# Optimization experiments

Measured on AMD Instinct MI355X. Metric: run time of the kernel, lower is better.

Reference implementation:

```python
import jax, jax.numpy as jnp
import numpy as np

HIDDEN = 512
HEADS = 8
HEAD_DIM = HIDDEN // HEADS


def setup_inputs() -> dict:
    key = jax.random.key(0)
    ks = jax.random.split(key, 9)
    B, S = 4, 2048
    scale = 1.0 / np.sqrt(HIDDEN)
    x = jax.random.normal(ks[0], (B, S, HIDDEN), dtype=jnp.float32)
    Wq = jax.random.normal(ks[1], (HIDDEN, HIDDEN), dtype=jnp.float32) * scale
    Wk = jax.random.normal(ks[2], (HIDDEN, HIDDEN), dtype=jnp.float32) * scale
    Wv = jax.random.normal(ks[3], (HIDDEN, HIDDEN), dtype=jnp.float32) * scale
    Wo = jax.random.normal(ks[4], (HIDDEN, HIDDEN), dtype=jnp.float32) * scale
    bq = jax.random.normal(ks[5], (HIDDEN,), dtype=jnp.float32) * 0.01
    bk = jax.random.normal(ks[6], (HIDDEN,), dtype=jnp.float32) * 0.01
    bv = jax.random.normal(ks[7], (HIDDEN,), dtype=jnp.float32) * 0.01
    bo = jax.random.normal(ks[8], (HIDDEN,), dtype=jnp.float32) * 0.01
    return {"x": x, "Wq": Wq, "bq": bq, "Wk": Wk, "bk": bk,
            "Wv": Wv, "bv": bv, "Wo": Wo, "bo": bo}


def reference(x, Wq, bq, Wk, bk, Wv, bv, Wo, bo):
    B, S, _ = x.shape
    # project and split heads: [B, H, S, D]
    def split_heads(t):
        return t.reshape(B, S, HEADS, HEAD_DIM).transpose(0, 2, 1, 3)
    Q = split_heads(x @ Wq.T + bq)
    K = split_heads(x @ Wk.T + bk)
    V = split_heads(x @ Wv.T + bv)
    scores = jnp.einsum("bhsd,bhtd->bhst", Q, K) / jnp.sqrt(
        jnp.array(HEAD_DIM, dtype=x.dtype))
    attn = jax.nn.softmax(scores, axis=-1)  # dropout is identity in eval
    ctx = jnp.einsum("bhst,bhtd->bhsd", attn, V)
    ctx = ctx.transpose(0, 2, 1, 3).reshape(B, S, HIDDEN)
    return ctx @ Wo.T + bo
```

## Files before the change

### kernel.cpp

```cpp
#include <hip/hip_runtime.h>
#include <stdint.h>

#define HID 512
#define NH 8
#define HD 64
#define BB 4
#define SS 2048

typedef unsigned short u16;
typedef __attribute__((ext_vector_type(8))) short short8;
typedef __attribute__((ext_vector_type(4))) float f32x4;
typedef __attribute__((ext_vector_type(4))) _Float16 f16x4;
typedef __attribute__((ext_vector_type(2))) unsigned int uint2v;

#define MFMA16(a, b, c) __builtin_amdgcn_mfma_f32_16x16x32_bf16((a), (b), (c), 0, 0, 0)
#define MFMAH16(a, b, c) __builtin_amdgcn_mfma_f32_16x16x16f16((a), (b), (c), 0, 0, 0)

#define WAIT_VM4() __builtin_amdgcn_s_waitcnt(0xF74)
#define WAIT_VM3() __builtin_amdgcn_s_waitcnt(0xF73)
#define WAIT_VM0() __builtin_amdgcn_s_waitcnt(0xF70)
#define PIPE_BARRIER() do { asm volatile("" ::: "memory"); \
  __builtin_amdgcn_s_barrier(); asm volatile("" ::: "memory"); } while (0)

__device__ __forceinline__ u16 f2bf(float f) {
  union { float f; uint32_t u; } v; v.f = f;
  return (u16)((v.u + 0x7fffu + ((v.u >> 16) & 1u)) >> 16);
}

__device__ __forceinline__ u16 f2h(float f) {
  _Float16 h = (_Float16)f;
  return __builtin_bit_cast(u16, h);
}

__device__ __forceinline__ void gl_lds16(const u16* g, u16* l) {
  __builtin_amdgcn_global_load_lds(
      (const __attribute__((address_space(1))) unsigned int*)g,
      (__attribute__((address_space(3))) unsigned int*)l, 16, 0, 0);
}

__global__ void prep(const float* __restrict__ x,
                     const float* __restrict__ w0, const float* __restrict__ w1,
                     const float* __restrict__ w2, const float* __restrict__ w3,
                     u16* __restrict__ xb,
                     u16* __restrict__ o0, u16* __restrict__ o1,
                     u16* __restrict__ o2, u16* __restrict__ o3) {
  const int bid = blockIdx.x;
  const float* in;
  u16* out;
  int base;
  if (bid < 4096) {
    in = x; out = xb; base = bid * 1024;
  } else {
    const int z = (bid - 4096) >> 8;
    base = ((bid - 4096) & 255) * 1024;
    in = (z == 0) ? w0 : (z == 1) ? w1 : (z == 2) ? w2 : w3;
    out = (z == 0) ? o0 : (z == 1) ? o1 : (z == 2) ? o2 : o3;
  }
  const int i = base + threadIdx.x * 4;
  float4 v = *(const float4*)(in + i);
  ushort4 o;
  o.x = f2bf(v.x); o.y = f2bf(v.y); o.z = f2bf(v.z); o.w = f2bf(v.w);
  *(ushort4*)(out + i) = o;
}

__global__ __launch_bounds__(256, 3)
void qkv_gemm(const u16* __restrict__ xb,
              const u16* __restrict__ wq, const u16* __restrict__ wk, const u16* __restrict__ wv,
              const float* __restrict__ bq, const float* __restrict__ bk, const float* __restrict__ bv,
              u16* __restrict__ Q, u16* __restrict__ K, u16* __restrict__ Vt) {
  __shared__ u16 sA[3][4096];
  __shared__ u16 sB[3][4096];
  const int tid = threadIdx.x;
  const int lane = tid & 63;
  const int wave = tid >> 6;
  const int l15 = lane & 15;
  const int quad = lane >> 4;
  const int wm = wave >> 1, wn = wave & 1;

  const int L = blockIdx.x;
  const int xcd = L & 7;
  const int slot = L >> 3;
  const int bm = xcd * 8 + (slot & 7);
  const int r2 = slot >> 3;
  const int bn = r2 & 3;
  const int z = r2 >> 2;

  const float* bias = (z == 0) ? bq : (z == 1) ? bk : bv;
  const float scale = (z == 0) ? 0.18033688011112042f : 1.0f;

  const u16* Arows = (z == 2) ? wv : xb;
  const u16* Brows = (z == 2) ? xb : ((z == 0) ? wq : wk);
  const int am0 = (z == 2) ? (bn * 128) : (bm * 128);
  const int bn0 = (z == 2) ? (bm * 128) : (bn * 128);

  const int srow = tid >> 2;
  const int sg = (tid & 3) ^ ((srow >> 1) & 3);
  const u16* gA = Arows + (am0 + srow) * 512 + sg * 8;
  const u16* gB = Brows + (bn0 + srow) * 512 + sg * 8;

  const int fsw = (quad ^ ((l15 >> 1) & 3)) * 8;
  int aoff[4], boff[4];
#pragma unroll
  for (int t = 0; t < 4; ++t) {
    aoff[t] = (wm * 64 + t * 16 + l15) * 32 + fsw;
    boff[t] = (wn * 64 + t * 16 + l15) * 32 + fsw;
  }

  f32x4 acc[4][4] = {};

#pragma unroll
  for (int t = 0; t < 2; ++t) {
    const int k0 = t * 32;
    gl_lds16(gA + k0, &sA[t][wave * 512]);
    gl_lds16(gA + k0 + 64 * 512, &sA[t][2048 + wave * 512]);
    gl_lds16(gB + k0, &sB[t][wave * 512]);
    gl_lds16(gB + k0 + 64 * 512, &sB[t][2048 + wave * 512]);
  }

  for (int kk = 0; kk < 16; ++kk) {
    WAIT_VM4();
    PIPE_BARRIER();
    {
      const int tp = (kk + 2 < 16) ? kk + 2 : 15;
      const int ns = (kk + 2) % 3;
      const int k0 = tp * 32;
      gl_lds16(gA + k0, &sA[ns][wave * 512]);
      gl_lds16(gA + k0 + 64 * 512, &sA[ns][2048 + wave * 512]);
      gl_lds16(gB + k0, &sB[ns][wave * 512]);
      gl_lds16(gB + k0 + 64 * 512, &sB[ns][2048 + wave * 512]);
    }
    const int cur = kk % 3;
    short8 af[4], bf[4];
#pragma unroll
    for (int t = 0; t < 4; ++t) af[t] = *(const short8*)&sA[cur][aoff[t]];
#pragma unroll
    for (int t = 0; t < 4; ++t) bf[t] = *(const short8*)&sB[cur][boff[t]];
#pragma unroll
    for (int mi = 0; mi < 4; ++mi)
#pragma unroll
      for (int ni = 0; ni < 4; ++ni)
        acc[mi][ni] = MFMA16(af[mi], bf[ni], acc[mi][ni]);
  }

  if (z != 2) {
    u16* dst = (z == 0) ? Q : K;
#pragma unroll
    for (int mi = 0; mi < 4; ++mi) {
#pragma unroll
      for (int ni = 0; ni < 4; ++ni) {
        const int col = bn0 + wn * 64 + ni * 16 + l15;
        const float bs = bias[col];
#pragma unroll
        for (int i = 0; i < 4; ++i) {
          const int row = am0 + wm * 64 + mi * 16 + quad * 4 + i;
          const float v = (acc[mi][ni][i] + bs) * scale;
          const int b = row >> 11, s = row & 2047;
          const int h = col >> 6, d = col & 63;
          dst[(((size_t)(b * 8 + h) * 2048 + s) << 6) + d] = f2bf(v);
        }
      }
    }
  } else {
#pragma unroll
    for (int mi = 0; mi < 4; ++mi) {
#pragma unroll
      for (int i = 0; i < 4; ++i) {
        const int o = am0 + wm * 64 + mi * 16 + quad * 4 + i;
        const float bs = bias[o];
        const int h = o >> 6, d = o & 63;
#pragma unroll
        for (int ni = 0; ni < 4; ++ni) {
          const int r = bn0 + wn * 64 + ni * 16 + l15;
          const int b = r >> 11, s = r & 2047;
          Vt[(((size_t)(b * 8 + h) * 64 + d) << 11) + s] = f2h(acc[mi][ni][i] + bs);
        }
      }
    }
  }
}

__global__ __launch_bounds__(512, 4)
void attn(const u16* __restrict__ Q, const u16* __restrict__ K,
          const u16* __restrict__ Vt, u16* __restrict__ ctx) {
  __shared__ __align__(16) u16 smem[4 * 8192];
  const int tid = threadIdx.x;
  const int lane = tid & 63;
  const int wave = tid >> 6;
  const int l15 = lane & 15;
  const int quad = lane >> 4;
  const int pair = wave >> 1;
  const int par = wave & 1;

  const int L = blockIdx.x;
  const int xcd = L & 7;
  const int slotb = L >> 3;
  const int bh = xcd * 4 + (slotb & 3);
  const int qt = slotb >> 2;

  const u16* Qb = Q + (size_t)bh * SS * HD;
  const u16* Kb = K + (size_t)bh * SS * HD;
  const u16* Vb = Vt + (size_t)bh * HD * SS;

  const int rowbase = qt * 128 + pair * 32;
  short8 qf[2][2];
#pragma unroll
  for (int rf = 0; rf < 2; ++rf)
#pragma unroll
    for (int kc = 0; kc < 2; ++kc)
      qf[rf][kc] = *(const short8*)(Qb + (rowbase + rf * 16 + l15) * 64 + kc * 32 + quad * 8);
  asm volatile("" ::: "memory");

  f32x4 oacc[2][4] = {};
  float plsum[2] = {0.f, 0.f};

  const int trow = tid >> 3;
  const int gsw = (tid & 7) ^ (trow & 7);
  const int kOff = trow * 64 + gsw * 8;
  const int vOff = trow * 2048 + gsw * 8;
  u16* ldsK = smem + tid * 8;
  u16* ldsV = smem + 4096 + tid * 8;

  const int l7 = l15 & 7;
  int kfo[2];
#pragma unroll
  for (int kc = 0; kc < 2; ++kc)
    kfo[kc] = (par * 32 + l15) * 64 + ((kc * 4 + quad) ^ l7) * 8;
  int vfo[2];
#pragma unroll
  for (int tb = 0; tb < 2; ++tb)
    vfo[tb] = l15 * 64 + (((par * 4 + tb * 2 + (quad >> 1)) ^ l7) * 8) + (quad & 1) * 4;

#pragma unroll
  for (int t = 0; t < 3; ++t) {
    gl_lds16(Kb + t * 4096 + kOff, ldsK + t * 8192);
    gl_lds16(Vb + t * 64 + vOff, ldsV + t * 8192);
  }

  for (int tt = 0; tt < 32; ++tt) {
    WAIT_VM4();
    PIPE_BARRIER();
    {
      const int tp = (tt + 3 < 32) ? tt + 3 : 31;
      const int ns = (tt + 3) & 3;
      gl_lds16(Kb + tp * 4096 + kOff, ldsK + ns * 8192);
      gl_lds16(Vb + tp * 64 + vOff, ldsV + ns * 8192);
    }
    const int cb = (tt & 3) * 8192;

#pragma unroll
    for (int tb = 0; tb < 2; ++tb) {
      const short8 k0 = *(const short8*)&smem[cb + tb * 1024 + kfo[0]];
      const short8 k1 = *(const short8*)&smem[cb + tb * 1024 + kfo[1]];
      f32x4 sacc[2] = {};
#pragma unroll
      for (int rf = 0; rf < 2; ++rf) {
        sacc[rf] = MFMA16(k0, qf[rf][0], sacc[rf]);
        sacc[rf] = MFMA16(k1, qf[rf][1], sacc[rf]);
      }
      uint2v vf[4];
#pragma unroll
      for (int nd = 0; nd < 4; ++nd)
        vf[nd] = *(const uint2v*)&smem[cb + 4096 + nd * 1024 + vfo[tb]];
#pragma unroll
      for (int rf = 0; rf < 2; ++rf) {
        const float p0 = __builtin_amdgcn_exp2f(sacc[rf][0]);
        const float p1 = __builtin_amdgcn_exp2f(sacc[rf][1]);
        const float p2 = __builtin_amdgcn_exp2f(sacc[rf][2]);
        const float p3 = __builtin_amdgcn_exp2f(sacc[rf][3]);
        plsum[rf] += (p0 + p1) + (p2 + p3);
        uint2v pu;
        pu.x = __builtin_bit_cast(unsigned int, __builtin_amdgcn_cvt_pkrtz(p0, p1));
        pu.y = __builtin_bit_cast(unsigned int, __builtin_amdgcn_cvt_pkrtz(p2, p3));
        const f16x4 pf = __builtin_bit_cast(f16x4, pu);
#pragma unroll
        for (int nd = 0; nd < 4; ++nd)
          oacc[rf][nd] = MFMAH16(pf, __builtin_bit_cast(f16x4, vf[nd]), oacc[rf][nd]);
      }
    }
  }

  WAIT_VM0();
  __syncthreads();

#pragma unroll
  for (int rf = 0; rf < 2; ++rf) {
    plsum[rf] += __shfl_xor(plsum[rf], 16);
    plsum[rf] += __shfl_xor(plsum[rf], 32);
  }

  float* cbuf = (float*)smem;
  float* lbuf = cbuf + 128 * 68;
  if (par) {
#pragma unroll
    for (int rf = 0; rf < 2; ++rf) {
#pragma unroll
      for (int nd = 0; nd < 4; ++nd)
#pragma unroll
        for (int i = 0; i < 4; ++i)
          cbuf[(pair * 32 + rf * 16 + quad * 4 + i) * 68 + nd * 16 + l15] = oacc[rf][nd][i];
      if (quad == 0) lbuf[pair * 32 + rf * 16 + l15] = plsum[rf];
    }
  }
  __syncthreads();
  if (!par) {
    const int b = bh >> 3, h = bh & 7;
#pragma unroll
    for (int rf = 0; rf < 2; ++rf) {
      const float tot = plsum[rf] + lbuf[pair * 32 + rf * 16 + l15];
      float inv[4];
#pragma unroll
      for (int i = 0; i < 4; ++i)
        inv[i] = __builtin_amdgcn_rcpf(__shfl(tot, quad * 4 + i));
#pragma unroll
      for (int nd = 0; nd < 4; ++nd)
#pragma unroll
        for (int i = 0; i < 4; ++i) {
          const float v = (oacc[rf][nd][i] +
                           cbuf[(pair * 32 + rf * 16 + quad * 4 + i) * 68 + nd * 16 + l15]) * inv[i];
          const int s = rowbase + rf * 16 + quad * 4 + i;
          const int d = nd * 16 + l15;
          ctx[((size_t)(b * 2048 + s) << 9) + h * 64 + d] = f2bf(v);
        }
    }
  }
}

__global__ __launch_bounds__(256, 2)
void out_gemm(const u16* __restrict__ A, const u16* __restrict__ W,
              const float* __restrict__ bias, float* __restrict__ out) {
  __shared__ u16 sA[3][4096];
  __shared__ u16 sB[3][2048];
  const int tid = threadIdx.x;
  const int lane = tid & 63;
  const int wave = tid >> 6;
  const int l15 = lane & 15;
  const int quad = lane >> 4;

  const int L = blockIdx.x;
  const int xcd = L & 7;
  const int slot = L >> 3;
  const int bm = xcd * 8 + (slot & 7);
  const int bn = slot >> 3;

  const int srow = tid >> 2;
  const int sg = (tid & 3) ^ ((srow >> 1) & 3);
  const u16* gA = A + (bm * 128 + srow) * 512 + sg * 8;
  const u16* gB = W + (bn * 64 + srow) * 512 + sg * 8;

  const int fsw = (quad ^ ((l15 >> 1) & 3)) * 8;
  int aoff[2], boff[4];
#pragma unroll
  for (int t = 0; t < 2; ++t) aoff[t] = (wave * 32 + t * 16 + l15) * 32 + fsw;
#pragma unroll
  for (int t = 0; t < 4; ++t) boff[t] = (t * 16 + l15) * 32 + fsw;

  f32x4 acc[2][4] = {};

#pragma unroll
  for (int t = 0; t < 2; ++t) {
    const int k0 = t * 32;
    gl_lds16(gA + k0, &sA[t][wave * 512]);
    gl_lds16(gA + k0 + 64 * 512, &sA[t][2048 + wave * 512]);
    gl_lds16(gB + k0, &sB[t][wave * 512]);
  }

  for (int kk = 0; kk < 16; ++kk) {
    WAIT_VM3();
    PIPE_BARRIER();
    {
      const int tp = (kk + 2 < 16) ? kk + 2 : 15;
      const int ns = (kk + 2) % 3;
      const int k0 = tp * 32;
      gl_lds16(gA + k0, &sA[ns][wave * 512]);
      gl_lds16(gA + k0 + 64 * 512, &sA[ns][2048 + wave * 512]);
      gl_lds16(gB + k0, &sB[ns][wave * 512]);
    }
    const int cur = kk % 3;
    short8 af[2], bf[4];
#pragma unroll
    for (int t = 0; t < 2; ++t) af[t] = *(const short8*)&sA[cur][aoff[t]];
#pragma unroll
    for (int t = 0; t < 4; ++t) bf[t] = *(const short8*)&sB[cur][boff[t]];
#pragma unroll
    for (int mi = 0; mi < 2; ++mi)
#pragma unroll
      for (int ni = 0; ni < 4; ++ni)
        acc[mi][ni] = MFMA16(af[mi], bf[ni], acc[mi][ni]);
  }

#pragma unroll
  for (int mi = 0; mi < 2; ++mi) {
#pragma unroll
    for (int ni = 0; ni < 4; ++ni) {
      const int col = bn * 64 + ni * 16 + l15;
      const float bs = bias[col];
#pragma unroll
      for (int i = 0; i < 4; ++i) {
        const int row = bm * 128 + wave * 32 + mi * 16 + quad * 4 + i;
        out[(size_t)row * 512 + col] = acc[mi][ni][i] + bs;
      }
    }
  }
}

extern "C" void kernel_launch(void* const* d_in, const int* in_sizes, int n_in,
                              void* d_out, int out_size, void* d_ws, size_t ws_size,
                              hipStream_t stream) {
  const float* x = (const float*)d_in[0];
  const float* Wq = (const float*)d_in[1];
  const float* bq = (const float*)d_in[2];
  const float* Wk = (const float*)d_in[3];
  const float* bk = (const float*)d_in[4];
  const float* Wv = (const float*)d_in[5];
  const float* bv = (const float*)d_in[6];
  const float* Wo = (const float*)d_in[7];
  const float* bo = (const float*)d_in[8];
  float* out = (float*)d_out;

  char* ws = (char*)d_ws;
  u16* xb  = (u16*)(ws);
  u16* wqb = (u16*)(ws + (8u << 20));
  u16* wkb = (u16*)(ws + (8u << 20) + (512u << 10));
  u16* wvb = (u16*)(ws + (9u << 20));
  u16* wob = (u16*)(ws + (9u << 20) + (512u << 10));
  u16* Qb  = (u16*)(ws + (10u << 20));
  u16* Kb  = (u16*)(ws + (18u << 20));
  u16* Vtb = (u16*)(ws + (26u << 20));
  u16* ctx = (u16*)(ws + (34u << 20));

  prep<<<5120, 256, 0, stream>>>(x, Wq, Wk, Wv, Wo, xb, wqb, wkb, wvb, wob);
  qkv_gemm<<<768, 256, 0, stream>>>(xb, wqb, wkb, wvb, bq, bk, bv, Qb, Kb, Vtb);
  attn<<<512, 512, 0, stream>>>(Qb, Kb, Vtb, ctx);
  out_gemm<<<512, 256, 0, stream>>>(ctx, wob, bo, out);
}
```

Baseline: 156.4 us.

## Restructure attention into per-wave K pipelines with V loaded into registers

```diff
diff --git a/kernel.cpp b/kernel.cpp
--- a/kernel.cpp
+++ b/kernel.cpp
@@ -19,8 +19,8 @@
 #define WAIT_VM4() __builtin_amdgcn_s_waitcnt(0xF74)
 #define WAIT_VM3() __builtin_amdgcn_s_waitcnt(0xF73)
 #define WAIT_VM0() __builtin_amdgcn_s_waitcnt(0xF70)
-#define PIPE_BARRIER() do { asm volatile("" ::: "memory"); \
-  __builtin_amdgcn_s_barrier(); asm volatile("" ::: "memory"); } while (0)
+#define FENCE() asm volatile("" ::: "memory")
+#define PIPE_BARRIER() do { FENCE(); __builtin_amdgcn_s_barrier(); FENCE(); } while (0)
 
 __device__ __forceinline__ u16 f2bf(float f) {
   union { float f; uint32_t u; } v; v.f = f;
@@ -179,10 +179,10 @@
   }
 }
 
-__global__ __launch_bounds__(512, 4)
+__global__ __launch_bounds__(256, 4)
 void attn(const u16* __restrict__ Q, const u16* __restrict__ K,
           const u16* __restrict__ Vt, u16* __restrict__ ctx) {
-  __shared__ __align__(16) u16 smem[4 * 8192];
+  __shared__ __align__(16) u16 smem[4 * 4096];
   const int tid = threadIdx.x;
   const int lane = tid & 63;
   const int wave = tid >> 6;
@@ -201,72 +201,83 @@
   const u16* Kb = K + (size_t)bh * SS * HD;
   const u16* Vb = Vt + (size_t)bh * HD * SS;
 
-  const int rowbase = qt * 128 + pair * 32;
+  const int rowbase = qt * 64 + pair * 32;
   short8 qf[2][2];
 #pragma unroll
   for (int rf = 0; rf < 2; ++rf)
 #pragma unroll
     for (int kc = 0; kc < 2; ++kc)
       qf[rf][kc] = *(const short8*)(Qb + (rowbase + rf * 16 + l15) * 64 + kc * 32 + quad * 8);
-  asm volatile("" ::: "memory");
 
   f32x4 oacc[2][4] = {};
   float plsum[2] = {0.f, 0.f};
 
-  const int trow = tid >> 3;
-  const int gsw = (tid & 7) ^ (trow & 7);
-  const int kOff = trow * 64 + gsw * 8;
-  const int vOff = trow * 2048 + gsw * 8;
-  u16* ldsK = smem + tid * 8;
-  u16* ldsV = smem + 4096 + tid * 8;
+  const int krho = lane >> 3;
+  const int kdg = (lane & 7) ^ krho;
+  const u16* ksrc = Kb + (par * 32 + krho) * 64 + kdg * 8;
+  u16* kdst = smem + wave * 4096 + lane * 8;
 
   const int l7 = l15 & 7;
-  int kfo[2];
-#pragma unroll
-  for (int kc = 0; kc < 2; ++kc)
-    kfo[kc] = (par * 32 + l15) * 64 + ((kc * 4 + quad) ^ l7) * 8;
-  int vfo[2];
+  int kfo[2][2];
 #pragma unroll
   for (int tb = 0; tb < 2; ++tb)
-    vfo[tb] = l15 * 64 + (((par * 4 + tb * 2 + (quad >> 1)) ^ l7) * 8) + (quad & 1) * 4;
-
-#pragma unroll
-  for (int t = 0; t < 3; ++t) {
-    gl_lds16(Kb + t * 4096 + kOff, ldsK + t * 8192);
-    gl_lds16(Vb + t * 64 + vOff, ldsV + t * 8192);
-  }
+#pragma unroll
+    for (int kc = 0; kc < 2; ++kc)
+      kfo[tb][kc] = wave * 4096 + (tb * 16 + l15) * 64 + ((kc * 4 + quad) ^ l7) * 8;
+
+  const u16* vsrc = Vb + l15 * 2048 + par * 32 + quad * 4;
+
+#define ISSUE_K(tile, slot)                                                   \
+  do {                                                                        \
+    _Pragma("unroll") for (int c = 0; c < 4; ++c)                             \
+      gl_lds16(ksrc + (size_t)(tile) * 4096 + c * 512,                        \
+               kdst + (slot) * 2048 + c * 512);                               \
+  } while (0)
+
+#define ISSUE_V(vreg, tile)                                                   \
+  do {                                                                        \
+    _Pragma("unroll") for (int tb = 0; tb < 2; ++tb)                          \
+      _Pragma("unroll") for (int nd = 0; nd < 4; ++nd)                        \
+        vreg[tb][nd] = *(const uint2v*)(vsrc + nd * 32768 + tb * 16 +         \
+                                        (size_t)(tile) * 64);                 \
+  } while (0)
+
+  uint2v vf[2][4];
+  ISSUE_K(0, 0);
+  ISSUE_K(1, 1);
+  ISSUE_V(vf, 0);
+  WAIT_VM0();
+  FENCE();
 
   for (int tt = 0; tt < 32; ++tt) {
-    WAIT_VM4();
-    PIPE_BARRIER();
-    {
-      const int tp = (tt + 3 < 32) ? tt + 3 : 31;
-      const int ns = (tt + 3) & 3;
-      gl_lds16(Kb + tp * 4096 + kOff, ldsK + ns * 8192);
-      gl_lds16(Vb + tp * 64 + vOff, ldsV + ns * 8192);
-    }
-    const int cb = (tt & 3) * 8192;
-
+    const int cs = (tt & 1) * 2048;
+
+    f32x4 sacc[2][2];
 #pragma unroll
     for (int tb = 0; tb < 2; ++tb) {
-      const short8 k0 = *(const short8*)&smem[cb + tb * 1024 + kfo[0]];
-      const short8 k1 = *(const short8*)&smem[cb + tb * 1024 + kfo[1]];
-      f32x4 sacc[2] = {};
+      const short8 k0 = *(const short8*)&smem[cs + kfo[tb][0]];
+      const short8 k1 = *(const short8*)&smem[cs + kfo[tb][1]];
 #pragma unroll
       for (int rf = 0; rf < 2; ++rf) {
-        sacc[rf] = MFMA16(k0, qf[rf][0], sacc[rf]);
-        sacc[rf] = MFMA16(k1, qf[rf][1], sacc[rf]);
+        f32x4 s = {};
+        s = MFMA16(k0, qf[rf][0], s);
+        s = MFMA16(k1, qf[rf][1], s);
+        sacc[tb][rf] = s;
       }
-      uint2v vf[4];
-#pragma unroll
-      for (int nd = 0; nd < 4; ++nd)
-        vf[nd] = *(const uint2v*)&smem[cb + 4096 + nd * 1024 + vfo[tb]];
+    }
+
+    FENCE();
+    WAIT_VM0();
+    FENCE();
+
+#pragma unroll
+    for (int tb = 0; tb < 2; ++tb) {
 #pragma unroll
       for (int rf = 0; rf < 2; ++rf) {
-        const float p0 = __builtin_amdgcn_exp2f(sacc[rf][0]);
-        const float p1 = __builtin_amdgcn_exp2f(sacc[rf][1]);
-        const float p2 = __builtin_amdgcn_exp2f(sacc[rf][2]);
-        const float p3 = __builtin_amdgcn_exp2f(sacc[rf][3]);
+        const float p0 = __builtin_amdgcn_exp2f(sacc[tb][rf][0]);
+        const float p1 = __builtin_amdgcn_exp2f(sacc[tb][rf][1]);
+        const float p2 = __builtin_amdgcn_exp2f(sacc[tb][rf][2]);
+        const float p3 = __builtin_amdgcn_exp2f(sacc[tb][rf][3]);
         plsum[rf] += (p0 + p1) + (p2 + p3);
         uint2v pu;
         pu.x = __builtin_bit_cast(unsigned int, __builtin_amdgcn_cvt_pkrtz(p0, p1));
@@ -274,9 +285,13 @@
         const f16x4 pf = __builtin_bit_cast(f16x4, pu);
 #pragma unroll
         for (int nd = 0; nd < 4; ++nd)
-          oacc[rf][nd] = MFMAH16(pf, __builtin_bit_cast(f16x4, vf[nd]), oacc[rf][nd]);
+          oacc[rf][nd] = MFMAH16(pf, __builtin_bit_cast(f16x4, vf[tb][nd]), oacc[rf][nd]);
       }
     }
+
+    if (tt < 30) ISSUE_K(tt + 2, tt & 1);
+    if (tt < 31) ISSUE_V(vf, tt + 1);
+    FENCE();
   }
 
   WAIT_VM0();
@@ -289,7 +304,7 @@
   }
 
   float* cbuf = (float*)smem;
-  float* lbuf = cbuf + 128 * 68;
+  float* lbuf = cbuf + 64 * 68;
   if (par) {
 #pragma unroll
     for (int rf = 0; rf < 2; ++rf) {
@@ -430,6 +445,6 @@
 
   prep<<<5120, 256, 0, stream>>>(x, Wq, Wk, Wv, Wo, xb, wqb, wkb, wvb, wob);
   qkv_gemm<<<768, 256, 0, stream>>>(xb, wqb, wkb, wvb, bq, bk, bv, Qb, Kb, Vtb);
-  attn<<<512, 512, 0, stream>>>(Qb, Kb, Vtb, ctx);
+  attn<<<1024, 256, 0, stream>>>(Qb, Kb, Vtb, ctx);
   out_gemm<<<512, 256, 0, stream>>>(ctx, wob, bo, out);
 }
```

Result: slower. 248.2 us (+58.7%).

## Software-pipeline QK^T of next tile with softmax and PV of current tile

Applied to the files above, without the earlier changes.

```diff
diff --git a/kernel.cpp b/kernel.cpp
--- a/kernel.cpp
+++ b/kernel.cpp
@@ -18,9 +18,10 @@
 
 #define WAIT_VM4() __builtin_amdgcn_s_waitcnt(0xF74)
 #define WAIT_VM3() __builtin_amdgcn_s_waitcnt(0xF73)
+#define WAIT_VM2() __builtin_amdgcn_s_waitcnt(0xF72)
 #define WAIT_VM0() __builtin_amdgcn_s_waitcnt(0xF70)
-#define PIPE_BARRIER() do { asm volatile("" ::: "memory"); \
-  __builtin_amdgcn_s_barrier(); asm volatile("" ::: "memory"); } while (0)
+#define FENCE() asm volatile("" ::: "memory")
+#define PIPE_BARRIER() do { FENCE(); __builtin_amdgcn_s_barrier(); FENCE(); } while (0)
 
 __device__ __forceinline__ u16 f2bf(float f) {
   union { float f; uint32_t u; } v; v.f = f;
@@ -208,7 +209,7 @@
 #pragma unroll
     for (int kc = 0; kc < 2; ++kc)
       qf[rf][kc] = *(const short8*)(Qb + (rowbase + rf * 16 + l15) * 64 + kc * 32 + quad * 8);
-  asm volatile("" ::: "memory");
+  FENCE();
 
   f32x4 oacc[2][4] = {};
   float plsum[2] = {0.f, 0.f};
@@ -235,38 +236,60 @@
     gl_lds16(Kb + t * 4096 + kOff, ldsK + t * 8192);
     gl_lds16(Vb + t * 64 + vOff, ldsV + t * 8192);
   }
+  WAIT_VM2();
+  PIPE_BARRIER();
+
+  f32x4 sacc[2][2][2];
+
+#pragma unroll
+  for (int tb = 0; tb < 2; ++tb) {
+    const short8 k0 = *(const short8*)&smem[tb * 1024 + kfo[0]];
+    const short8 k1 = *(const short8*)&smem[tb * 1024 + kfo[1]];
+#pragma unroll
+    for (int rf = 0; rf < 2; ++rf) {
+      f32x4 s = {};
+      s = MFMA16(k0, qf[rf][0], s);
+      s = MFMA16(k1, qf[rf][1], s);
+      sacc[0][tb][rf] = s;
+    }
+  }
 
   for (int tt = 0; tt < 32; ++tt) {
-    WAIT_VM4();
-    PIPE_BARRIER();
+    const int pp = tt & 1;
+    const int cbC = (tt & 3) * 8192;
+    const int cbN = ((tt + 1) & 3) * 8192;
+
+    if (tt > 0) PIPE_BARRIER();
     {
       const int tp = (tt + 3 < 32) ? tt + 3 : 31;
       const int ns = (tt + 3) & 3;
       gl_lds16(Kb + tp * 4096 + kOff, ldsK + ns * 8192);
       gl_lds16(Vb + tp * 64 + vOff, ldsV + ns * 8192);
     }
-    const int cb = (tt & 3) * 8192;
 
 #pragma unroll
     for (int tb = 0; tb < 2; ++tb) {
-      const short8 k0 = *(const short8*)&smem[cb + tb * 1024 + kfo[0]];
-      const short8 k1 = *(const short8*)&smem[cb + tb * 1024 + kfo[1]];
-      f32x4 sacc[2] = {};
-#pragma unroll
-      for (int rf = 0; rf < 2; ++rf) {
-        sacc[rf] = MFMA16(k0, qf[rf][0], sacc[rf]);
-        sacc[rf] = MFMA16(k1, qf[rf][1], sacc[rf]);
+      if (tt < 31) {
+        const short8 k0 = *(const short8*)&smem[cbN + tb * 1024 + kfo[0]];
+        const short8 k1 = *(const short8*)&smem[cbN + tb * 1024 + kfo[1]];
+#pragma unroll
+        for (int rf = 0; rf < 2; ++rf) {
+          f32x4 s = {};
+          s = MFMA16(k0, qf[rf][0], s);
+          s = MFMA16(k1, qf[rf][1], s);
+          sacc[pp ^ 1][tb][rf] = s;
+        }
       }
       uint2v vf[4];
 #pragma unroll
       for (int nd = 0; nd < 4; ++nd)
-        vf[nd] = *(const uint2v*)&smem[cb + 4096 + nd * 1024 + vfo[tb]];
+        vf[nd] = *(const uint2v*)&smem[cbC + 4096 + nd * 1024 + vfo[tb]];
 #pragma unroll
       for (int rf = 0; rf < 2; ++rf) {
-        const float p0 = __builtin_amdgcn_exp2f(sacc[rf][0]);
-        const float p1 = __builtin_amdgcn_exp2f(sacc[rf][1]);
-        const float p2 = __builtin_amdgcn_exp2f(sacc[rf][2]);
-        const float p3 = __builtin_amdgcn_exp2f(sacc[rf][3]);
+        const float p0 = __builtin_amdgcn_exp2f(sacc[pp][tb][rf][0]);
+        const float p1 = __builtin_amdgcn_exp2f(sacc[pp][tb][rf][1]);
+        const float p2 = __builtin_amdgcn_exp2f(sacc[pp][tb][rf][2]);
+        const float p3 = __builtin_amdgcn_exp2f(sacc[pp][tb][rf][3]);
         plsum[rf] += (p0 + p1) + (p2 + p3);
         uint2v pu;
         pu.x = __builtin_bit_cast(unsigned int, __builtin_amdgcn_cvt_pkrtz(p0, p1));
@@ -277,6 +300,7 @@
           oacc[rf][nd] = MFMAH16(pf, __builtin_bit_cast(f16x4, vf[nd]), oacc[rf][nd]);
       }
     }
+    WAIT_VM2();
   }
 
   WAIT_VM0();
```

Result: slower. 161.6 us (+3.4%).
